# Optimization experiments

Hardware: AMD Instinct MI355X
Metric: run time of the kernel (lower is better)

## Reference

```python
import jax, jax.numpy as jnp
import numpy as np

B, D, H, C, T = 65536, 512, 256, 100, 10
EPS = 0.01  # halt_epsilon


def setup_inputs() -> dict:
    key = jax.random.key(0)
    ks = jax.random.split(key, 10)
    sD = 1.0 / np.sqrt(D)
    sH = 1.0 / np.sqrt(H)
    return {
        "x": jax.random.normal(ks[0], (B, D), dtype=jnp.float32),
        # GRUCell params (PyTorch layout: rows chunked as [r; z; n])
        "W_ih": jax.random.uniform(ks[1], (3 * H, D), minval=-sD, maxval=sD, dtype=jnp.float32),
        "W_hh": jax.random.uniform(ks[2], (3 * H, H), minval=-sH, maxval=sH, dtype=jnp.float32),
        "b_ih": jax.random.uniform(ks[3], (3 * H,), minval=-sH, maxval=sH, dtype=jnp.float32),
        "b_hh": jax.random.uniform(ks[4], (3 * H,), minval=-sH, maxval=sH, dtype=jnp.float32),
        # halting unit
        "W_halt": jax.random.uniform(ks[5], (1, H), minval=-sH, maxval=sH, dtype=jnp.float32),
        "b_halt": jax.random.uniform(ks[6], (1,), minval=-sH, maxval=sH, dtype=jnp.float32),
        # readout
        "W_ro": jax.random.uniform(ks[7], (C, H), minval=-sH, maxval=sH, dtype=jnp.float32),
        "b_ro": jax.random.uniform(ks[8], (C,), minval=-sH, maxval=sH, dtype=jnp.float32),
    }


def _act_forward(x, W_ih, W_hh, b_ih, b_hh, W_halt, b_halt, W_ro, b_ro):
    dt = x.dtype
    thresh = jnp.asarray(1.0 - EPS, dt)
    # x is static across ponder steps -> precompute input projection once
    x_proj = x @ W_ih.T + b_ih                       # [B, 3H]
    xr, xz, xn = jnp.split(x_proj, 3, axis=-1)

    def step(carry, _):
        h, cum, rem, nup, acc = carry
        h_proj = h @ W_hh.T + b_hh                   # [B, 3H]
        hr, hz, hn = jnp.split(h_proj, 3, axis=-1)
        r = jax.nn.sigmoid(xr + hr)
        z = jax.nn.sigmoid(xz + hz)
        n = jnp.tanh(xn + r * hn)
        h_new = (1.0 - z) * n + z * h                # GRUCell update
        halt = jax.nn.sigmoid(h_new @ W_halt.T + b_halt)[:, 0]  # [B]
        logits_t = h_new @ W_ro.T + b_ro             # [B, C]
        still = (cum < thresh).astype(dt)
        new_halt = halt * still
        would = (cum + new_halt > thresh).astype(dt)
        remainder = (1.0 - cum) * would * still
        step_w = new_halt * (1.0 - would) + remainder
        cum2 = cum + step_w
        acc2 = acc + step_w[:, None] * h_new
        return (h_new, cum2, rem + remainder, nup + still, acc2), (h_new, halt, logits_t)

    zB = jnp.zeros((x.shape[0],), dt)
    init = (jnp.zeros((x.shape[0], W_hh.shape[1]), dt), zB, zB, zB,
            jnp.zeros((x.shape[0], W_hh.shape[1]), dt))
    (h, cum, remainders, n_updates, acc), (h_seq, halt_seq, logits_seq) = jax.lax.scan(
        step, init, None, length=T)
    logits = acc @ W_ro.T + b_ro                     # [B, C]
    ponder_cost = n_updates.mean() + remainders.mean()
    # scan stacks on axis 0 (time) -> move to dim 1 as torch.stack(dim=1)
    h_seq = jnp.swapaxes(h_seq, 0, 1)                # [B, T, H]
    halt_seq = jnp.swapaxes(halt_seq, 0, 1)          # [B, T]
    logits_seq = jnp.swapaxes(logits_seq, 0, 1)      # [B, T, C]
    return logits, ponder_cost, n_updates, h_seq, halt_seq, logits_seq


def reference(x, W_ih, W_hh, b_ih, b_hh, W_halt, b_halt, W_ro, b_ro):
    return _act_forward(x, W_ih, W_hh, b_ih, b_hh, W_halt, b_halt, W_ro, b_ro)
```

## Files before the change

kernel.cpp:

```cpp
#include <hip/hip_runtime.h>
#include <cmath>


namespace {
constexpr int B = 65536, D = 512, H = 256, C = 100, T = 10;

constexpr long OUT_LOGITS = 0;
constexpr long OUT_PONDER = (long)B * C;
constexpr long OUT_NUP    = OUT_PONDER + 1;
constexpr long OUT_HSEQ   = OUT_NUP + B;
constexpr long OUT_HALT   = OUT_HSEQ + (long)B * T * H;
constexpr long OUT_LSEQ   = OUT_HALT + (long)B * T;

constexpr long NIH  = 768L * D;
constexpr long NHH  = 768L * H;
constexpr long NAUG = 112L * H;

constexpr long WS_XP   = 0;
constexpr long WS_W16  = WS_XP + (long)B * 768;
constexpr long W_HALV  = 2 * (NIH + NHH + NAUG);
constexpr long WS_HL   = WS_W16 + (W_HALV + 1) / 2;
constexpr long WS_HP4  = WS_HL + (long)B * T;
constexpr long WS_NUPB = WS_HP4 + 4L * B * T;
constexpr long WS_REMB = WS_NUPB + B;
constexpr long WS_H16  = WS_REMB + B;
constexpr long H16_PER_T = 1024L * 32768;

constexpr float SC  = 256.f;
constexpr float ISC = 1.f / 256.f;
constexpr float SB  = 1.f / 65536.f;
}

typedef __attribute__((ext_vector_type(8))) _Float16 h8;
typedef __attribute__((ext_vector_type(4))) _Float16 h4;
typedef __attribute__((ext_vector_type(4))) float f4;

#define MFMA16(A, Bo, Cc) __builtin_amdgcn_mfma_f32_16x16x32_f16(A, Bo, Cc, 0, 0, 0)
#define PROD3(a, Ah, Al, Bh, Bl)                                               \
  a = MFMA16(Al, Bh, a);                                                       \
  a = MFMA16(Ah, Bl, a);                                                       \
  a = MFMA16(Ah, Bh, a);

__device__ __forceinline__ float sigmoidf_(float x) {
  if (x >= 0.f) { return 1.f / (1.f + expf(-x)); }
  float e = expf(x);
  return e / (1.f + e);
}

__device__ __forceinline__ void gload_lds16(const _Float16* g, _Float16* l) {
  __builtin_amdgcn_global_load_lds(
      (const __attribute__((address_space(1))) unsigned int*)g,
      (__attribute__((address_space(3))) unsigned int*)l, 16, 0, 0);
}

__global__ void k_prep(const float* __restrict__ wih_s, const float* __restrict__ whh_s,
                       const float* __restrict__ wro, const float* __restrict__ whalt,
                       _Float16* __restrict__ wr) {
  long idx = (long)blockIdx.x * 256 + threadIdx.x;
  if (idx < NIH) {
    float xs = wih_s[idx] * SC;
    _Float16 h = (_Float16)xs;
    _Float16 l = (_Float16)(xs - (float)h);
    wr[idx] = h; wr[NIH + idx] = l;
  }
  if (idx < NHH) {
    float xs = whh_s[idx] * SC;
    _Float16 h = (_Float16)xs;
    _Float16 l = (_Float16)(xs - (float)h);
    long b = 2 * NIH;
    wr[b + idx] = h; wr[b + NHH + idx] = l;
  }
  if (idx < NAUG) {
    int row = (int)(idx >> 8), k = (int)(idx & 255);
    float x = (row < C) ? wro[row * 256 + k] : ((row == C) ? whalt[k] : 0.f);
    float xs = x * SC;
    _Float16 h = (_Float16)xs;
    _Float16 l = (_Float16)(xs - (float)h);
    long b = 2 * (NIH + NHH);
    wr[b + idx] = h; wr[b + NAUG + idx] = l;
  }
}

__device__ __forceinline__ void stageA16(const float* __restrict__ src,
                                         _Float16* As0, _Float16* As1,
                                         int o) {
#pragma unroll
  for (int i = 0; i < 4; ++i) {
    float4 v = ((const float4*)src)[i];
    float vv[4] = {v.x, v.y, v.z, v.w};
    h4 hh, ll;
#pragma unroll
    for (int c = 0; c < 4; ++c) {
      float sv = vv[c] * SC;
      _Float16 h = (_Float16)sv;
      hh[c] = h;
      ll[c] = (_Float16)(sv - (float)h);
    }
    *(h4*)&As0[o + i * 4] = hh;
    *(h4*)&As1[o + i * 4] = ll;
  }
}

__global__ __launch_bounds__(256, 3) void k_xproj(
    const float* __restrict__ x, const _Float16* __restrict__ wih,
    const float* __restrict__ b_ih, float* __restrict__ xp) {
  __shared__ __align__(16) _Float16 As0[128 * 40], As1[128 * 40];
  __shared__ __align__(16) _Float16 Bs[2][192 * 32];
  const int tid = threadIdx.x;
  const int w = tid >> 6, l = tid & 63;
  const int lr = l & 15, lq = l >> 4;
  const int bid = blockIdx.x;
  const int gid = (bid & 7) * 256 + (bid >> 3);
  const int c0 = (gid & 3) * 64;
  const int rb = (gid >> 2) * 128;

  f4 acc[8][3];
#pragma unroll
  for (int i = 0; i < 8; ++i)
#pragma unroll
    for (int g = 0; g < 3; ++g) acc[i][g] = (f4)0.f;

  for (int kc = 0; kc < 16; ++kc) {
    const int k0 = kc * 32;
    __syncthreads();
    {
      const int row = tid >> 1, kk0 = (tid & 1) * 16;
      stageA16(x + (long)(rb + row) * D + k0 + kk0, As0, As1, row * 40 + kk0);
    }
#pragma unroll
    for (int j = 0; j < 6; ++j) {
      int chunk = w * 6 + j;
      int plane = chunk / 12;
      int rem = chunk - plane * 12;
      int scol = rem * 16 + (l >> 2);
      int kq = l & 3;
      int gcol = (scol >> 6) * 256 + c0 + (scol & 63);
      gload_lds16(wih + (long)plane * NIH + (long)gcol * D + k0 + kq * 8,
                  &Bs[plane][rem * 512]);
    }
    __syncthreads();
    h8 Bh[3], Bl[3];
#pragma unroll
    for (int g = 0; g < 3; ++g) {
      Bh[g] = *(const h8*)&Bs[0][(g * 64 + w * 16 + lr) * 32 + lq * 8];
      Bl[g] = *(const h8*)&Bs[1][(g * 64 + w * 16 + lr) * 32 + lq * 8];
    }
#pragma unroll
    for (int i = 0; i < 8; ++i) {
      h8 Ah = *(const h8*)&As0[(i * 16 + lr) * 40 + lq * 8];
      h8 Al = *(const h8*)&As1[(i * 16 + lr) * 40 + lq * 8];
#pragma unroll
      for (int g = 0; g < 3; ++g) { PROD3(acc[i][g], Ah, Al, Bh[g], Bl[g]); }
    }
  }
  const int ch = c0 + w * 16 + lr;
  float bi[3] = {b_ih[ch], b_ih[256 + ch], b_ih[512 + ch]};
#pragma unroll
  for (int i = 0; i < 8; ++i)
#pragma unroll
    for (int g = 0; g < 3; ++g)
#pragma unroll
      for (int reg = 0; reg < 4; ++reg) {
        long row = rb + i * 16 + lq * 4 + reg;
        xp[row * 768 + g * 256 + ch] = fmaf(acc[i][g][reg], SB, bi[g]);
      }
}

__global__ __launch_bounds__(256, 4) void k_gru(
    const _Float16* __restrict__ whh, const float* __restrict__ xp,
    const float* __restrict__ b_hh, const float* __restrict__ w_halt,
    float* __restrict__ out, _Float16* __restrict__ h16,
    float* __restrict__ hp4, int t) {
  __shared__ __align__(16) _Float16 As[2][64 * 32];
  __shared__ __align__(16) _Float16 Bs[2][192 * 32];
  __shared__ float lds_hp[64][4];
  const int tid = threadIdx.x;
  const int w = tid >> 6, l = tid & 63;
  const int lr = l & 15, lq = l >> 4;
  const int bid = blockIdx.x;
  const int gid = (bid & 7) * 512 + (bid >> 3);
  const int strip = gid & 3;
  const int c0 = strip * 64;
  const int rb = (gid >> 2) * 64;
  const long tilebase = (long)(rb >> 6) * 32768;
  const int ch = c0 + w * 16 + lr;
  const int kc_h = ch >> 5;

  f4 acc[4][3];
  float ho[4][4];
#pragma unroll
  for (int i = 0; i < 4; ++i) {
#pragma unroll
    for (int reg = 0; reg < 4; ++reg) {
      long row = rb + i * 16 + lq * 4 + reg;
      acc[i][0][reg] = xp[row * 768 + ch] * 65536.f;
      acc[i][1][reg] = xp[row * 768 + 256 + ch] * 65536.f;
      ho[i][reg] = 0.f;
    }
    acc[i][2] = (f4)0.f;
  }

  if (t > 0) {
    const _Float16* h16r = h16 + (long)(t - 1) * H16_PER_T + tilebase;
    for (int kc = 0; kc < 8; ++kc) {
      const int k0 = kc * 32;
      __syncthreads();
#pragma unroll
      for (int j = 0; j < 2; ++j) {
        int c = w * 2 + j;
        int plane = c >> 2;
        int cc = c & 3;
        gload_lds16(h16r + (long)kc * 4096 + plane * 2048 + cc * 512 + l * 8,
                    &As[plane][cc * 512]);
      }
#pragma unroll
      for (int j = 0; j < 6; ++j) {
        int chunk = w * 6 + j;
        int plane = chunk / 12;
        int rem = chunk - plane * 12;
        int scol = rem * 16 + (l >> 2);
        int kq = l & 3;
        int gcol = (scol >> 6) * 256 + c0 + (scol & 63);
        gload_lds16(whh + (long)plane * NHH + (long)gcol * H + k0 + kq * 8,
                    &Bs[plane][rem * 512]);
      }
      __syncthreads();
      h8 Bh[3], Bl[3];
#pragma unroll
      for (int g = 0; g < 3; ++g) {
        Bh[g] = *(const h8*)&Bs[0][(g * 64 + w * 16 + lr) * 32 + lq * 8];
        Bl[g] = *(const h8*)&Bs[1][(g * 64 + w * 16 + lr) * 32 + lq * 8];
      }
#pragma unroll
      for (int i = 0; i < 4; ++i) {
        h8 Ah = *(const h8*)&As[0][(i * 16 + lr) * 32 + lq * 8];
        h8 Al = *(const h8*)&As[1][(i * 16 + lr) * 32 + lq * 8];
#pragma unroll
        for (int g = 0; g < 3; ++g) { PROD3(acc[i][g], Ah, Al, Bh[g], Bl[g]); }
      }
      if (kc == kc_h) {
#pragma unroll
        for (int i = 0; i < 4; ++i)
#pragma unroll
          for (int reg = 0; reg < 4; ++reg) {
            int rloc = i * 16 + lq * 4 + reg;
            ho[i][reg] = ((float)As[0][rloc * 32 + (ch & 31)] +
                          (float)As[1][rloc * 32 + (ch & 31)]) * ISC;
          }
      }
    }
  }

  const float bhr = b_hh[ch], bhz = b_hh[256 + ch], bhn = b_hh[512 + ch];
  const float whv = w_halt[ch];
  const long h16base = (long)t * H16_PER_T + tilebase + (long)kc_h * 4096 + (ch & 31);
#pragma unroll
  for (int i = 0; i < 4; ++i)
#pragma unroll
    for (int reg = 0; reg < 4; ++reg) {
      const int rloc = i * 16 + lq * 4 + reg;
      const long row = rb + rloc;
      float xn = xp[row * 768 + 512 + ch];
      float rr = sigmoidf_(fmaf(acc[i][0][reg], SB, bhr));
      float zz = sigmoidf_(fmaf(acc[i][1][reg], SB, bhz));
      float nn = tanhf(xn + rr * fmaf(acc[i][2][reg], SB, bhn));
      float hv = (1.f - zz) * nn + zz * ho[i][reg];
      out[OUT_HSEQ + row * (T * H) + (long)t * H + ch] = hv;
      float sv = hv * SC;
      _Float16 hi = (_Float16)sv;
      _Float16 lo = (_Float16)(sv - (float)hi);
      h16[h16base + (long)rloc * 32] = hi;
      h16[h16base + 2048 + (long)rloc * 32] = lo;
      float p = hv * whv;
#pragma unroll
      for (int m = 1; m < 16; m <<= 1) p += __shfl_xor(p, m, 64);
      if (lr == 0) lds_hp[rloc][w] = p;
    }
  __syncthreads();
  if (tid < 64)
    hp4[((long)t * 4 + strip) * B + rb + tid] =
        ((lds_hp[tid][0] + lds_hp[tid][1]) + (lds_hp[tid][2] + lds_hp[tid][3]));
}

__global__ __launch_bounds__(256, 4) void k_lseq(
    const _Float16* __restrict__ h16, const _Float16* __restrict__ waug,
    const float* __restrict__ b_ro, float* __restrict__ lseq) {
  __shared__ __align__(16) _Float16 As[128 * 32];
  __shared__ __align__(16) _Float16 Bs[112 * 32];
  const int tid = threadIdx.x;
  const int w = tid >> 6, l = tid & 63;
  const int lr = l & 15, lq = l >> 4;
  const int t = blockIdx.x >> 9;
  const int btile = blockIdx.x & 511;
  const _Float16* h16r = h16 + (long)t * H16_PER_T + (long)btile * 65536;

  f4 acc[2][7];
#pragma unroll
  for (int i = 0; i < 2; ++i)
#pragma unroll
    for (int j = 0; j < 7; ++j) acc[i][j] = (f4)0.f;

  for (int kc = 0; kc < 8; ++kc) {
    const int k0 = kc * 32;
    __syncthreads();
#pragma unroll
    for (int j = 0; j < 2; ++j) {
      int c = w * 2 + j;
      gload_lds16(h16r + (long)(c >> 2) * 32768 + (long)kc * 4096 + (c & 3) * 512 + l * 8,
                  &As[c * 512]);
    }
#pragma unroll
    for (int j = 0; j < 2; ++j) {
      int chunk = w + j * 4;
      if (chunk < 7) {
        int scol = chunk * 16 + (l >> 2);
        int kq = l & 3;
        gload_lds16(waug + (long)scol * H + k0 + kq * 8, &Bs[chunk * 512]);
      }
    }
    __syncthreads();
    h8 Af[2];
#pragma unroll
    for (int i = 0; i < 2; ++i)
      Af[i] = *(const h8*)&As[(w * 32 + i * 16 + lr) * 32 + lq * 8];
#pragma unroll
    for (int j = 0; j < 7; ++j) {
      h8 Bf = *(const h8*)&Bs[(j * 16 + lr) * 32 + lq * 8];
#pragma unroll
      for (int i = 0; i < 2; ++i) acc[i][j] = MFMA16(Af[i], Bf, acc[i][j]);
    }
  }
#pragma unroll
  for (int j = 0; j < 7; ++j) {
    const int col = j * 16 + lr;
    if (col < C) {
      const float br = b_ro[col];
#pragma unroll
      for (int i = 0; i < 2; ++i)
#pragma unroll
        for (int reg = 0; reg < 4; ++reg) {
          long b = (long)btile * 128 + w * 32 + i * 16 + lq * 4 + reg;
          lseq[(b * T + t) * C + col] = fmaf(acc[i][j][reg], SB, br);
        }
    }
  }
}

__global__ void k_act(const float* __restrict__ hp4, const float* __restrict__ b_halt,
                      float* __restrict__ out, float* __restrict__ swb,
                      float* __restrict__ nupb, float* __restrict__ remb) {
  const long b = (long)blockIdx.x * 256 + threadIdx.x;
  const float bh = b_halt[0];
  float cum = 0.f, rem = 0.f, nu = 0.f;
#pragma unroll
  for (int t = 0; t < T; ++t) {
    float v = bh + hp4[((long)t * 4 + 0) * B + b] + hp4[((long)t * 4 + 1) * B + b] +
              hp4[((long)t * 4 + 2) * B + b] + hp4[((long)t * 4 + 3) * B + b];
    float halt = sigmoidf_(v);
    out[OUT_HALT + b * T + t] = halt;
    float still = (cum < 0.99f) ? 1.f : 0.f;
    float nh = halt * still;
    float would = ((cum + nh) > 0.99f) ? 1.f : 0.f;
    float rema = (1.f - cum) * would * still;
    float swv = nh * (1.f - would) + rema;
    cum += swv; rem += rema; nu += still;
    swb[b * T + t] = swv;
  }
  nupb[b] = nu; remb[b] = rem;
}

__global__ void k_logits(const float* __restrict__ lseq, const float* __restrict__ swb,
                         const float* __restrict__ b_ro, const float* __restrict__ nupb,
                         float* __restrict__ out) {
  const long b = blockIdx.x;
  const int tid = threadIdx.x;
  if (tid < C) {
    float br = b_ro[tid];
    float s = br;
#pragma unroll
    for (int t = 0; t < T; ++t) {
      float sw = swb[b * T + t];
      s = fmaf(sw, lseq[(b * T + t) * C + tid] - br, s);
    }
    out[OUT_LOGITS + b * C + tid] = s;
  } else if (tid == C) {
    out[OUT_NUP + b] = nupb[b];
  }
}

__global__ void k_ponder(const float* __restrict__ nupb, const float* __restrict__ remb,
                         float* __restrict__ out) {
  __shared__ float sm[4];
  float s = 0.f;
  for (int i = threadIdx.x; i < B; i += 256) s += nupb[i] + remb[i];
#pragma unroll
  for (int m = 1; m < 64; m <<= 1) s += __shfl_xor(s, m, 64);
  int w = threadIdx.x >> 6;
  if ((threadIdx.x & 63) == 0) sm[w] = s;
  __syncthreads();
  if (threadIdx.x == 0)
    out[OUT_PONDER] = (sm[0] + sm[1] + sm[2] + sm[3]) * (1.f / (float)B);
}

extern "C" void kernel_launch(void* const* d_in, const int* in_sizes, int n_in,
                              void* d_out, int out_size, void* d_ws, size_t ws_size,
                              hipStream_t stream) {
  const float* x      = (const float*)d_in[0];
  const float* W_ih   = (const float*)d_in[1];
  const float* W_hh   = (const float*)d_in[2];
  const float* b_ih   = (const float*)d_in[3];
  const float* b_hh   = (const float*)d_in[4];
  const float* W_halt = (const float*)d_in[5];
  const float* b_halt = (const float*)d_in[6];
  const float* W_ro   = (const float*)d_in[7];
  const float* b_ro   = (const float*)d_in[8];
  float* out = (float*)d_out;
  float* ws  = (float*)d_ws;

  float* xp        = ws + WS_XP;
  _Float16* w16    = (_Float16*)(ws + WS_W16);
  _Float16* wih16  = w16;
  _Float16* whh16  = w16 + 2 * NIH;
  _Float16* waug16 = w16 + 2 * (NIH + NHH);
  float* swb  = ws + WS_HL;
  float* hp4  = ws + WS_HP4;
  float* nupb = ws + WS_NUPB;
  float* remb = ws + WS_REMB;
  _Float16* h16 = (_Float16*)(ws + WS_H16);

  k_prep<<<(int)((NIH + 255) / 256), 256, 0, stream>>>(W_ih, W_hh, W_ro, W_halt, w16);
  k_xproj<<<2048, 256, 0, stream>>>(x, wih16, b_ih, xp);
  for (int t = 0; t < T; ++t)
    k_gru<<<4096, 256, 0, stream>>>(whh16, xp, b_hh, W_halt, out, h16, hp4, t);
  k_lseq<<<512 * T, 256, 0, stream>>>(h16, waug16, b_ro, out + OUT_LSEQ);
  k_act<<<B / 256, 256, 0, stream>>>(hp4, b_halt, out, swb, nupb, remb);
  k_logits<<<B, 128, 0, stream>>>(out + OUT_LSEQ, swb, b_ro, nupb, out);
  k_ponder<<<1, 256, 0, stream>>>(nupb, remb, out);
}
```

Measured before the change: 2.192 ms.

## Fuse all GRU timesteps and ACT halting into one persistent row-tile kernel

The ten per-timestep GRU launches are replaced by a single kernel. Each block owns a 64-row tile and loops over all timesteps and all four hidden-column strips, reading back the fp16 hidden state it wrote itself in the previous step. The ACT halting recurrence now runs inside that kernel using shared-memory accumulators, so the separate k_act launch and the hp4 intermediate buffer go away. The aim is to remove launch gaps, tail effects and global round-trips, at the cost of serialising the four column strips within each block and relying on exactly one wave of 1024 resident blocks.

```diff
diff --git a/kernel.cpp b/kernel.cpp
--- a/kernel.cpp
+++ b/kernel.cpp
@@ -20,8 +20,7 @@
 constexpr long WS_W16  = WS_XP + (long)B * 768;
 constexpr long W_HALV  = 2 * (NIH + NHH + NAUG);
 constexpr long WS_HL   = WS_W16 + (W_HALV + 1) / 2;
-constexpr long WS_HP4  = WS_HL + (long)B * T;
-constexpr long WS_NUPB = WS_HP4 + 4L * B * T;
+constexpr long WS_NUPB = WS_HL + (long)B * T;
 constexpr long WS_REMB = WS_NUPB + B;
 constexpr long WS_H16  = WS_REMB + B;
 constexpr long H16_PER_T = 1024L * 32768;
@@ -166,120 +165,154 @@
       }
 }
 
-__global__ __launch_bounds__(256, 4) void k_gru(
+__global__ __launch_bounds__(256, 4) void k_gru_all(
     const _Float16* __restrict__ whh, const float* __restrict__ xp,
     const float* __restrict__ b_hh, const float* __restrict__ w_halt,
-    float* __restrict__ out, _Float16* __restrict__ h16,
-    float* __restrict__ hp4, int t) {
+    const float* __restrict__ b_halt, float* __restrict__ out,
+    _Float16* __restrict__ h16, float* __restrict__ swb,
+    float* __restrict__ nupb, float* __restrict__ remb) {
   __shared__ __align__(16) _Float16 As[2][64 * 32];
   __shared__ __align__(16) _Float16 Bs[2][192 * 32];
   __shared__ float lds_hp[64][4];
+  __shared__ float lds_ss[64][4];
+  __shared__ float lds_cum[64], lds_rem[64], lds_nu[64];
   const int tid = threadIdx.x;
   const int w = tid >> 6, l = tid & 63;
   const int lr = l & 15, lq = l >> 4;
   const int bid = blockIdx.x;
-  const int gid = (bid & 7) * 512 + (bid >> 3);
-  const int strip = gid & 3;
-  const int c0 = strip * 64;
-  const int rb = (gid >> 2) * 64;
-  const long tilebase = (long)(rb >> 6) * 32768;
-  const int ch = c0 + w * 16 + lr;
-  const int kc_h = ch >> 5;
-
-  f4 acc[4][3];
-  float ho[4][4];
-#pragma unroll
-  for (int i = 0; i < 4; ++i) {
-#pragma unroll
-    for (int reg = 0; reg < 4; ++reg) {
-      long row = rb + i * 16 + lq * 4 + reg;
-      acc[i][0][reg] = xp[row * 768 + ch] * 65536.f;
-      acc[i][1][reg] = xp[row * 768 + 256 + ch] * 65536.f;
-      ho[i][reg] = 0.f;
-    }
-    acc[i][2] = (f4)0.f;
-  }
-
-  if (t > 0) {
-    const _Float16* h16r = h16 + (long)(t - 1) * H16_PER_T + tilebase;
-    for (int kc = 0; kc < 8; ++kc) {
-      const int k0 = kc * 32;
+  const int gid = (bid & 7) * 128 + (bid >> 3);
+  const int rb = gid * 64;
+  const long tilebase = (long)gid * 32768;
+  const float bh = b_halt[0];
+
+  if (tid < 64) { lds_cum[tid] = 0.f; lds_rem[tid] = 0.f; lds_nu[tid] = 0.f; }
+
+  for (int t = 0; t < T; ++t) {
+    for (int cs = 0; cs < 4; ++cs) {
+      const int c0 = cs * 64;
+      const int ch = c0 + w * 16 + lr;
+      const int kc_h = ch >> 5;
+
+      f4 acc[4][3];
+      float ho[4][4];
+#pragma unroll
+      for (int i = 0; i < 4; ++i) {
+#pragma unroll
+        for (int reg = 0; reg < 4; ++reg) {
+          long row = rb + i * 16 + lq * 4 + reg;
+          acc[i][0][reg] = xp[row * 768 + ch] * 65536.f;
+          acc[i][1][reg] = xp[row * 768 + 256 + ch] * 65536.f;
+          ho[i][reg] = 0.f;
+        }
+        acc[i][2] = (f4)0.f;
+      }
+
+      if (t > 0) {
+        const _Float16* h16r = h16 + (long)(t - 1) * H16_PER_T + tilebase;
+        for (int kc = 0; kc < 8; ++kc) {
+          const int k0 = kc * 32;
+          __syncthreads();
+#pragma unroll
+          for (int j = 0; j < 2; ++j) {
+            int c = w * 2 + j;
+            int plane = c >> 2;
+            int cc = c & 3;
+            gload_lds16(h16r + (long)kc * 4096 + plane * 2048 + cc * 512 + l * 8,
+                        &As[plane][cc * 512]);
+          }
+#pragma unroll
+          for (int j = 0; j < 6; ++j) {
+            int chunk = w * 6 + j;
+            int plane = chunk / 12;
+            int rem = chunk - plane * 12;
+            int scol = rem * 16 + (l >> 2);
+            int kq = l & 3;
+            int gcol = (scol >> 6) * 256 + c0 + (scol & 63);
+            gload_lds16(whh + (long)plane * NHH + (long)gcol * H + k0 + kq * 8,
+                        &Bs[plane][rem * 512]);
+          }
+          __syncthreads();
+          h8 Bh[3], Bl[3];
+#pragma unroll
+          for (int g = 0; g < 3; ++g) {
+            Bh[g] = *(const h8*)&Bs[0][(g * 64 + w * 16 + lr) * 32 + lq * 8];
+            Bl[g] = *(const h8*)&Bs[1][(g * 64 + w * 16 + lr) * 32 + lq * 8];
+          }
+#pragma unroll
+          for (int i = 0; i < 4; ++i) {
+            h8 Ah = *(const h8*)&As[0][(i * 16 + lr) * 32 + lq * 8];
+            h8 Al = *(const h8*)&As[1][(i * 16 + lr) * 32 + lq * 8];
+#pragma unroll
+            for (int g = 0; g < 3; ++g) { PROD3(acc[i][g], Ah, Al, Bh[g], Bl[g]); }
+          }
+          if (kc == kc_h) {
+#pragma unroll
+            for (int i = 0; i < 4; ++i)
+#pragma unroll
+              for (int reg = 0; reg < 4; ++reg) {
+                int rloc = i * 16 + lq * 4 + reg;
+                ho[i][reg] = ((float)As[0][rloc * 32 + (ch & 31)] +
+                              (float)As[1][rloc * 32 + (ch & 31)]) * ISC;
+              }
+          }
+        }
+      }
+
+      const float bhr = b_hh[ch], bhz = b_hh[256 + ch], bhn = b_hh[512 + ch];
+      const float whv = w_halt[ch];
+      const long h16base = (long)t * H16_PER_T + tilebase + (long)kc_h * 4096 + (ch & 31);
+#pragma unroll
+      for (int i = 0; i < 4; ++i)
+#pragma unroll
+        for (int reg = 0; reg < 4; ++reg) {
+          const int rloc = i * 16 + lq * 4 + reg;
+          const long row = rb + rloc;
+          float xn = xp[row * 768 + 512 + ch];
+          float rr = sigmoidf_(fmaf(acc[i][0][reg], SB, bhr));
+          float zz = sigmoidf_(fmaf(acc[i][1][reg], SB, bhz));
+          float nn = tanhf(xn + rr * fmaf(acc[i][2][reg], SB, bhn));
+          float hv = (1.f - zz) * nn + zz * ho[i][reg];
+          out[OUT_HSEQ + row * (T * H) + (long)t * H + ch] = hv;
+          float sv = hv * SC;
+          _Float16 hi = (_Float16)sv;
+          _Float16 lo = (_Float16)(sv - (float)hi);
+          h16[h16base + (long)rloc * 32] = hi;
+          h16[h16base + 2048 + (long)rloc * 32] = lo;
+          float p = hv * whv;
+#pragma unroll
+          for (int m = 1; m < 16; m <<= 1) p += __shfl_xor(p, m, 64);
+          if (lr == 0) lds_hp[rloc][w] = p;
+        }
       __syncthreads();
-#pragma unroll
-      for (int j = 0; j < 2; ++j) {
-        int c = w * 2 + j;
-        int plane = c >> 2;
-        int cc = c & 3;
-        gload_lds16(h16r + (long)kc * 4096 + plane * 2048 + cc * 512 + l * 8,
-                    &As[plane][cc * 512]);
-      }
-#pragma unroll
-      for (int j = 0; j < 6; ++j) {
-        int chunk = w * 6 + j;
-        int plane = chunk / 12;
-        int rem = chunk - plane * 12;
-        int scol = rem * 16 + (l >> 2);
-        int kq = l & 3;
-        int gcol = (scol >> 6) * 256 + c0 + (scol & 63);
-        gload_lds16(whh + (long)plane * NHH + (long)gcol * H + k0 + kq * 8,
-                    &Bs[plane][rem * 512]);
-      }
+      if (tid < 64)
+        lds_ss[tid][cs] =
+            (lds_hp[tid][0] + lds_hp[tid][1]) + (lds_hp[tid][2] + lds_hp[tid][3]);
       __syncthreads();
-      h8 Bh[3], Bl[3];
-#pragma unroll
-      for (int g = 0; g < 3; ++g) {
-        Bh[g] = *(const h8*)&Bs[0][(g * 64 + w * 16 + lr) * 32 + lq * 8];
-        Bl[g] = *(const h8*)&Bs[1][(g * 64 + w * 16 + lr) * 32 + lq * 8];
-      }
-#pragma unroll
-      for (int i = 0; i < 4; ++i) {
-        h8 Ah = *(const h8*)&As[0][(i * 16 + lr) * 32 + lq * 8];
-        h8 Al = *(const h8*)&As[1][(i * 16 + lr) * 32 + lq * 8];
-#pragma unroll
-        for (int g = 0; g < 3; ++g) { PROD3(acc[i][g], Ah, Al, Bh[g], Bl[g]); }
-      }
-      if (kc == kc_h) {
-#pragma unroll
-        for (int i = 0; i < 4; ++i)
-#pragma unroll
-          for (int reg = 0; reg < 4; ++reg) {
-            int rloc = i * 16 + lq * 4 + reg;
-            ho[i][reg] = ((float)As[0][rloc * 32 + (ch & 31)] +
-                          (float)As[1][rloc * 32 + (ch & 31)]) * ISC;
-          }
-      }
-    }
-  }
-
-  const float bhr = b_hh[ch], bhz = b_hh[256 + ch], bhn = b_hh[512 + ch];
-  const float whv = w_halt[ch];
-  const long h16base = (long)t * H16_PER_T + tilebase + (long)kc_h * 4096 + (ch & 31);
-#pragma unroll
-  for (int i = 0; i < 4; ++i)
-#pragma unroll
-    for (int reg = 0; reg < 4; ++reg) {
-      const int rloc = i * 16 + lq * 4 + reg;
-      const long row = rb + rloc;
-      float xn = xp[row * 768 + 512 + ch];
-      float rr = sigmoidf_(fmaf(acc[i][0][reg], SB, bhr));
-      float zz = sigmoidf_(fmaf(acc[i][1][reg], SB, bhz));
-      float nn = tanhf(xn + rr * fmaf(acc[i][2][reg], SB, bhn));
-      float hv = (1.f - zz) * nn + zz * ho[i][reg];
-      out[OUT_HSEQ + row * (T * H) + (long)t * H + ch] = hv;
-      float sv = hv * SC;
-      _Float16 hi = (_Float16)sv;
-      _Float16 lo = (_Float16)(sv - (float)hi);
-      h16[h16base + (long)rloc * 32] = hi;
-      h16[h16base + 2048 + (long)rloc * 32] = lo;
-      float p = hv * whv;
-#pragma unroll
-      for (int m = 1; m < 16; m <<= 1) p += __shfl_xor(p, m, 64);
-      if (lr == 0) lds_hp[rloc][w] = p;
-    }
-  __syncthreads();
-  if (tid < 64)
-    hp4[((long)t * 4 + strip) * B + rb + tid] =
-        ((lds_hp[tid][0] + lds_hp[tid][1]) + (lds_hp[tid][2] + lds_hp[tid][3]));
+    }
+
+    if (tid < 64) {
+      const long b = rb + tid;
+      float v = bh + lds_ss[tid][0] + lds_ss[tid][1] + lds_ss[tid][2] + lds_ss[tid][3];
+      float halt = sigmoidf_(v);
+      out[OUT_HALT + b * T + t] = halt;
+      float cum = lds_cum[tid];
+      float still = (cum < 0.99f) ? 1.f : 0.f;
+      float nh = halt * still;
+      float would = ((cum + nh) > 0.99f) ? 1.f : 0.f;
+      float rema = (1.f - cum) * would * still;
+      float swv = nh * (1.f - would) + rema;
+      lds_cum[tid] = cum + swv;
+      lds_rem[tid] += rema;
+      lds_nu[tid] += still;
+      swb[b * T + t] = swv;
+    }
+    __syncthreads();
+  }
+
+  if (tid < 64) {
+    nupb[rb + tid] = lds_nu[tid];
+    remb[rb + tid] = lds_rem[tid];
+  }
 }
 
 __global__ __launch_bounds__(256, 4) void k_lseq(
@@ -344,29 +377,6 @@
         }
     }
   }
-}
-
-__global__ void k_act(const float* __restrict__ hp4, const float* __restrict__ b_halt,
-                      float* __restrict__ out, float* __restrict__ swb,
-                      float* __restrict__ nupb, float* __restrict__ remb) {
-  const long b = (long)blockIdx.x * 256 + threadIdx.x;
-  const float bh = b_halt[0];
-  float cum = 0.f, rem = 0.f, nu = 0.f;
-#pragma unroll
-  for (int t = 0; t < T; ++t) {
-    float v = bh + hp4[((long)t * 4 + 0) * B + b] + hp4[((long)t * 4 + 1) * B + b] +
-              hp4[((long)t * 4 + 2) * B + b] + hp4[((long)t * 4 + 3) * B + b];
-    float halt = sigmoidf_(v);
-    out[OUT_HALT + b * T + t] = halt;
-    float still = (cum < 0.99f) ? 1.f : 0.f;
-    float nh = halt * still;
-    float would = ((cum + nh) > 0.99f) ? 1.f : 0.f;
-    float rema = (1.f - cum) * would * still;
-    float swv = nh * (1.f - would) + rema;
-    cum += swv; rem += rema; nu += still;
-    swb[b * T + t] = swv;
-  }
-  nupb[b] = nu; remb[b] = rem;
 }
 
 __global__ void k_logits(const float* __restrict__ lseq, const float* __restrict__ swb,
@@ -423,17 +433,15 @@
   _Float16* whh16  = w16 + 2 * NIH;
   _Float16* waug16 = w16 + 2 * (NIH + NHH);
   float* swb  = ws + WS_HL;
-  float* hp4  = ws + WS_HP4;
   float* nupb = ws + WS_NUPB;
   float* remb = ws + WS_REMB;
   _Float16* h16 = (_Float16*)(ws + WS_H16);
 
   k_prep<<<(int)((NIH + 255) / 256), 256, 0, stream>>>(W_ih, W_hh, W_ro, W_halt, w16);
   k_xproj<<<2048, 256, 0, stream>>>(x, wih16, b_ih, xp);
-  for (int t = 0; t < T; ++t)
-    k_gru<<<4096, 256, 0, stream>>>(whh16, xp, b_hh, W_halt, out, h16, hp4, t);
+  k_gru_all<<<1024, 256, 0, stream>>>(whh16, xp, b_hh, W_halt, b_halt, out, h16,
+                                      swb, nupb, remb);
   k_lseq<<<512 * T, 256, 0, stream>>>(h16, waug16, b_ro, out + OUT_LSEQ);
-  k_act<<<B / 256, 256, 0, stream>>>(hp4, b_halt, out, swb, nupb, remb);
   k_logits<<<B, 128, 0, stream>>>(out + OUT_LSEQ, swb, b_ro, nupb, out);
   k_ponder<<<1, 256, 0, stream>>>(nupb, remb, out);
 }
```

Result: slower. 4.029 ms (+83.8%).

## Fuse logits-seq GEMM with weighted logits reduction and swizzle LDS layouts

Applied to the files above, without the earlier changes.

Replaces the separate per-timestep readout GEMM and the logits reduction kernel with one kernel that loops over all timesteps per 64-row tile. It accumulates the step-weighted logits in registers, which avoids re-reading the large logits sequence. The nupdate output moves into the ACT kernel. Separately, it applies an XOR swizzle to the LDS layouts of the xproj, GRU and readout GEMMs to reduce bank conflicts on fragment reads. The fused kernel launches only 1024 blocks and runs the timesteps serially, which may reduce parallelism.

```diff
diff --git a/kernel.cpp b/kernel.cpp
--- a/kernel.cpp
+++ b/kernel.cpp
@@ -40,6 +40,9 @@
   a = MFMA16(Al, Bh, a);                                                       \
   a = MFMA16(Ah, Bl, a);                                                       \
   a = MFMA16(Ah, Bh, a);
+
+#define SWZ_L(l)  ((((l) & 3) ^ (((l) >> 3) & 3)) << 3)
+#define SWZ_RD(lq, lr) (((lq) ^ (((lr) >> 1) & 3)) << 3)
 
 __device__ __forceinline__ float sigmoidf_(float x) {
   if (x >= 0.f) { return 1.f / (1.f + expf(-x)); }
@@ -133,17 +136,16 @@
       int plane = chunk / 12;
       int rem = chunk - plane * 12;
       int scol = rem * 16 + (l >> 2);
-      int kq = l & 3;
       int gcol = (scol >> 6) * 256 + c0 + (scol & 63);
-      gload_lds16(wih + (long)plane * NIH + (long)gcol * D + k0 + kq * 8,
+      gload_lds16(wih + (long)plane * NIH + (long)gcol * D + k0 + SWZ_L(l),
                   &Bs[plane][rem * 512]);
     }
     __syncthreads();
     h8 Bh[3], Bl[3];
 #pragma unroll
     for (int g = 0; g < 3; ++g) {
-      Bh[g] = *(const h8*)&Bs[0][(g * 64 + w * 16 + lr) * 32 + lq * 8];
-      Bl[g] = *(const h8*)&Bs[1][(g * 64 + w * 16 + lr) * 32 + lq * 8];
+      Bh[g] = *(const h8*)&Bs[0][(g * 64 + w * 16 + lr) * 32 + SWZ_RD(lq, lr)];
+      Bl[g] = *(const h8*)&Bs[1][(g * 64 + w * 16 + lr) * 32 + SWZ_RD(lq, lr)];
     }
 #pragma unroll
     for (int i = 0; i < 8; ++i) {
@@ -210,7 +212,8 @@
         int c = w * 2 + j;
         int plane = c >> 2;
         int cc = c & 3;
-        gload_lds16(h16r + (long)kc * 4096 + plane * 2048 + cc * 512 + l * 8,
+        gload_lds16(h16r + (long)kc * 4096 + plane * 2048 + cc * 512 +
+                        (l >> 2) * 32 + SWZ_L(l),
                     &As[plane][cc * 512]);
       }
 #pragma unroll
@@ -219,22 +222,21 @@
         int plane = chunk / 12;
         int rem = chunk - plane * 12;
         int scol = rem * 16 + (l >> 2);
-        int kq = l & 3;
         int gcol = (scol >> 6) * 256 + c0 + (scol & 63);
-        gload_lds16(whh + (long)plane * NHH + (long)gcol * H + k0 + kq * 8,
+        gload_lds16(whh + (long)plane * NHH + (long)gcol * H + k0 + SWZ_L(l),
                     &Bs[plane][rem * 512]);
       }
       __syncthreads();
       h8 Bh[3], Bl[3];
 #pragma unroll
       for (int g = 0; g < 3; ++g) {
-        Bh[g] = *(const h8*)&Bs[0][(g * 64 + w * 16 + lr) * 32 + lq * 8];
-        Bl[g] = *(const h8*)&Bs[1][(g * 64 + w * 16 + lr) * 32 + lq * 8];
+        Bh[g] = *(const h8*)&Bs[0][(g * 64 + w * 16 + lr) * 32 + SWZ_RD(lq, lr)];
+        Bl[g] = *(const h8*)&Bs[1][(g * 64 + w * 16 + lr) * 32 + SWZ_RD(lq, lr)];
       }
 #pragma unroll
       for (int i = 0; i < 4; ++i) {
-        h8 Ah = *(const h8*)&As[0][(i * 16 + lr) * 32 + lq * 8];
-        h8 Al = *(const h8*)&As[1][(i * 16 + lr) * 32 + lq * 8];
+        h8 Ah = *(const h8*)&As[0][(i * 16 + lr) * 32 + SWZ_RD(lq, lr)];
+        h8 Al = *(const h8*)&As[1][(i * 16 + lr) * 32 + SWZ_RD(lq, lr)];
 #pragma unroll
         for (int g = 0; g < 3; ++g) { PROD3(acc[i][g], Ah, Al, Bh[g], Bl[g]); }
       }
@@ -244,8 +246,9 @@
 #pragma unroll
           for (int reg = 0; reg < 4; ++reg) {
             int rloc = i * 16 + lq * 4 + reg;
-            ho[i][reg] = ((float)As[0][rloc * 32 + (ch & 31)] +
-                          (float)As[1][rloc * 32 + (ch & 31)]) * ISC;
+            int sl = ((((ch >> 3) & 3) ^ ((rloc >> 1) & 3)) << 3) + (ch & 7);
+            ho[i][reg] = ((float)As[0][rloc * 32 + sl] +
+                          (float)As[1][rloc * 32 + sl]) * ISC;
           }
       }
     }
@@ -282,70 +285,6 @@
         ((lds_hp[tid][0] + lds_hp[tid][1]) + (lds_hp[tid][2] + lds_hp[tid][3]));
 }
 
-__global__ __launch_bounds__(256, 4) void k_lseq(
-    const _Float16* __restrict__ h16, const _Float16* __restrict__ waug,
-    const float* __restrict__ b_ro, float* __restrict__ lseq) {
-  __shared__ __align__(16) _Float16 As[128 * 32];
-  __shared__ __align__(16) _Float16 Bs[112 * 32];
-  const int tid = threadIdx.x;
-  const int w = tid >> 6, l = tid & 63;
-  const int lr = l & 15, lq = l >> 4;
-  const int t = blockIdx.x >> 9;
-  const int btile = blockIdx.x & 511;
-  const _Float16* h16r = h16 + (long)t * H16_PER_T + (long)btile * 65536;
-
-  f4 acc[2][7];
-#pragma unroll
-  for (int i = 0; i < 2; ++i)
-#pragma unroll
-    for (int j = 0; j < 7; ++j) acc[i][j] = (f4)0.f;
-
-  for (int kc = 0; kc < 8; ++kc) {
-    const int k0 = kc * 32;
-    __syncthreads();
-#pragma unroll
-    for (int j = 0; j < 2; ++j) {
-      int c = w * 2 + j;
-      gload_lds16(h16r + (long)(c >> 2) * 32768 + (long)kc * 4096 + (c & 3) * 512 + l * 8,
-                  &As[c * 512]);
-    }
-#pragma unroll
-    for (int j = 0; j < 2; ++j) {
-      int chunk = w + j * 4;
-      if (chunk < 7) {
-        int scol = chunk * 16 + (l >> 2);
-        int kq = l & 3;
-        gload_lds16(waug + (long)scol * H + k0 + kq * 8, &Bs[chunk * 512]);
-      }
-    }
-    __syncthreads();
-    h8 Af[2];
-#pragma unroll
-    for (int i = 0; i < 2; ++i)
-      Af[i] = *(const h8*)&As[(w * 32 + i * 16 + lr) * 32 + lq * 8];
-#pragma unroll
-    for (int j = 0; j < 7; ++j) {
-      h8 Bf = *(const h8*)&Bs[(j * 16 + lr) * 32 + lq * 8];
-#pragma unroll
-      for (int i = 0; i < 2; ++i) acc[i][j] = MFMA16(Af[i], Bf, acc[i][j]);
-    }
-  }
-#pragma unroll
-  for (int j = 0; j < 7; ++j) {
-    const int col = j * 16 + lr;
-    if (col < C) {
-      const float br = b_ro[col];
-#pragma unroll
-      for (int i = 0; i < 2; ++i)
-#pragma unroll
-        for (int reg = 0; reg < 4; ++reg) {
-          long b = (long)btile * 128 + w * 32 + i * 16 + lq * 4 + reg;
-          lseq[(b * T + t) * C + col] = fmaf(acc[i][j][reg], SB, br);
-        }
-    }
-  }
-}
-
 __global__ void k_act(const float* __restrict__ hp4, const float* __restrict__ b_halt,
                       float* __restrict__ out, float* __restrict__ swb,
                       float* __restrict__ nupb, float* __restrict__ remb) {
@@ -367,24 +306,84 @@
     swb[b * T + t] = swv;
   }
   nupb[b] = nu; remb[b] = rem;
-}
-
-__global__ void k_logits(const float* __restrict__ lseq, const float* __restrict__ swb,
-                         const float* __restrict__ b_ro, const float* __restrict__ nupb,
-                         float* __restrict__ out) {
-  const long b = blockIdx.x;
+  out[OUT_NUP + b] = nu;
+}
+
+__global__ __launch_bounds__(256, 4) void k_lseq2(
+    const _Float16* __restrict__ h16, const _Float16* __restrict__ waug,
+    const float* __restrict__ b_ro, const float* __restrict__ swb,
+    float* __restrict__ out) {
+  __shared__ __align__(16) _Float16 As[64 * 32];
+  __shared__ __align__(16) _Float16 Bs[112 * 32];
+  __shared__ float swf[640];
   const int tid = threadIdx.x;
-  if (tid < C) {
-    float br = b_ro[tid];
-    float s = br;
-#pragma unroll
-    for (int t = 0; t < T; ++t) {
-      float sw = swb[b * T + t];
-      s = fmaf(sw, lseq[(b * T + t) * C + tid] - br, s);
-    }
-    out[OUT_LOGITS + b * C + tid] = s;
-  } else if (tid == C) {
-    out[OUT_NUP + b] = nupb[b];
+  const int w = tid >> 6, l = tid & 63;
+  const int lr = l & 15, lq = l >> 4;
+  const long rb = (long)blockIdx.x * 64;
+  const long tilebase = (long)blockIdx.x * 32768;
+
+  for (int j = tid; j < 640; j += 256) swf[j] = swb[rb * T + j];
+
+  float br_[7];
+#pragma unroll
+  for (int j = 0; j < 7; ++j) {
+    int col = j * 16 + lr;
+    br_[j] = (col < C) ? b_ro[col] : 0.f;
+  }
+
+  f4 Lacc[7];
+#pragma unroll
+  for (int j = 0; j < 7; ++j) Lacc[j] = (f4)0.f;
+
+  for (int t = 0; t < T; ++t) {
+    const _Float16* h16t = h16 + (long)t * H16_PER_T + tilebase;
+    f4 acc[7];
+#pragma unroll
+    for (int j = 0; j < 7; ++j) acc[j] = (f4)0.f;
+
+    for (int kc = 0; kc < 8; ++kc) {
+      __syncthreads();
+      gload_lds16(h16t + (long)kc * 4096 + w * 512 + (l >> 2) * 32 + SWZ_L(l),
+                  &As[w * 512]);
+#pragma unroll
+      for (int j = 0; j < 2; ++j) {
+        int chunk = w + j * 4;
+        if (chunk < 7) {
+          int scol = chunk * 16 + (l >> 2);
+          gload_lds16(waug + (long)scol * H + kc * 32 + SWZ_L(l), &Bs[chunk * 512]);
+        }
+      }
+      __syncthreads();
+      h8 Af = *(const h8*)&As[(w * 16 + lr) * 32 + SWZ_RD(lq, lr)];
+#pragma unroll
+      for (int j = 0; j < 7; ++j) {
+        h8 Bf = *(const h8*)&Bs[(j * 16 + lr) * 32 + SWZ_RD(lq, lr)];
+        acc[j] = MFMA16(Af, Bf, acc[j]);
+      }
+    }
+#pragma unroll
+    for (int reg = 0; reg < 4; ++reg) {
+      const long m = rb + w * 16 + lq * 4 + reg;
+      const float swv = swf[(w * 16 + lq * 4 + reg) * 10 + t];
+#pragma unroll
+      for (int j = 0; j < 7; ++j) {
+        int col = j * 16 + lr;
+        if (col < C) {
+          out[OUT_LSEQ + (m * T + t) * C + col] = fmaf(acc[j][reg], SB, br_[j]);
+          Lacc[j][reg] = fmaf(swv, acc[j][reg], Lacc[j][reg]);
+        }
+      }
+    }
+  }
+#pragma unroll
+  for (int reg = 0; reg < 4; ++reg) {
+    const long m = rb + w * 16 + lq * 4 + reg;
+#pragma unroll
+    for (int j = 0; j < 7; ++j) {
+      int col = j * 16 + lr;
+      if (col < C)
+        out[OUT_LOGITS + m * C + col] = fmaf(Lacc[j][reg], SB, br_[j]);
+    }
   }
 }
 
@@ -432,8 +431,7 @@
   k_xproj<<<2048, 256, 0, stream>>>(x, wih16, b_ih, xp);
   for (int t = 0; t < T; ++t)
     k_gru<<<4096, 256, 0, stream>>>(whh16, xp, b_hh, W_halt, out, h16, hp4, t);
-  k_lseq<<<512 * T, 256, 0, stream>>>(h16, waug16, b_ro, out + OUT_LSEQ);
   k_act<<<B / 256, 256, 0, stream>>>(hp4, b_halt, out, swb, nupb, remb);
-  k_logits<<<B, 128, 0, stream>>>(out + OUT_LSEQ, swb, b_ro, nupb, out);
+  k_lseq2<<<1024, 256, 0, stream>>>(h16, waug16, b_ro, swb, out);
   k_ponder<<<1, 256, 0, stream>>>(nupb, remb, out);
 }
```

Measured after the change: 3.314 ms. 51.2% more time.

## Store input projection in MFMA-fragment-tiled layout for vectorized GRU loads

Applied to the files above, without the earlier changes.

The input projection buffer is rewritten in a tiled layout that matches the accumulator fragment ownership of each thread, so k_xproj writes float4s and k_gru reads r/z/n gate inputs as three float4 loads per row group. Before, each thread did scalar strided loads across 768-wide rows in every one of the ten GRU step launches. The n-gate input is now loaded up front into registers rather than in the epilogue, which raises register pressure slightly. Producer and consumer index maps must agree exactly.

```diff
diff --git a/kernel.cpp b/kernel.cpp
--- a/kernel.cpp
+++ b/kernel.cpp
@@ -103,7 +103,7 @@
 
 __global__ __launch_bounds__(256, 3) void k_xproj(
     const float* __restrict__ x, const _Float16* __restrict__ wih,
-    const float* __restrict__ b_ih, float* __restrict__ xp) {
+    const float* __restrict__ b_ih, float* __restrict__ xpt) {
   __shared__ __align__(16) _Float16 As0[128 * 40], As1[128 * 40];
   __shared__ __align__(16) _Float16 Bs[2][192 * 32];
   const int tid = threadIdx.x;
@@ -154,20 +154,25 @@
     }
   }
   const int ch = c0 + w * 16 + lr;
+  const int strip = gid & 3;
   float bi[3] = {b_ih[ch], b_ih[256 + ch], b_ih[512 + ch]};
-#pragma unroll
-  for (int i = 0; i < 8; ++i)
-#pragma unroll
-    for (int g = 0; g < 3; ++g)
-#pragma unroll
-      for (int reg = 0; reg < 4; ++reg) {
-        long row = rb + i * 16 + lq * 4 + reg;
-        xp[row * 768 + g * 256 + ch] = fmaf(acc[i][g][reg], SB, bi[g]);
-      }
+  const long xoff = (long)(lq * 256 + w * 64 + lr * 4);
+#pragma unroll
+  for (int i = 0; i < 8; ++i) {
+    const long t4s = (long)((gid >> 2) * 2 + (i >> 2)) * 4 + strip;
+#pragma unroll
+    for (int g = 0; g < 3; ++g) {
+      float4 v = make_float4(fmaf(acc[i][g][0], SB, bi[g]),
+                             fmaf(acc[i][g][1], SB, bi[g]),
+                             fmaf(acc[i][g][2], SB, bi[g]),
+                             fmaf(acc[i][g][3], SB, bi[g]));
+      *(float4*)&xpt[((t4s * 3 + g) * 4 + (i & 3)) * 1024 + xoff] = v;
+    }
+  }
 }
 
 __global__ __launch_bounds__(256, 4) void k_gru(
-    const _Float16* __restrict__ whh, const float* __restrict__ xp,
+    const _Float16* __restrict__ whh, const float* __restrict__ xpt,
     const float* __restrict__ b_hh, const float* __restrict__ w_halt,
     float* __restrict__ out, _Float16* __restrict__ h16,
     float* __restrict__ hp4, int t) {
@@ -188,16 +193,22 @@
 
   f4 acc[4][3];
   float ho[4][4];
+  float xnv[4][4];
+  const long t4s = (long)(gid >> 2) * 4 + strip;
+  const long xoff = (long)(lq * 256 + w * 64 + lr * 4);
 #pragma unroll
   for (int i = 0; i < 4; ++i) {
-#pragma unroll
-    for (int reg = 0; reg < 4; ++reg) {
-      long row = rb + i * 16 + lq * 4 + reg;
-      acc[i][0][reg] = xp[row * 768 + ch] * 65536.f;
-      acc[i][1][reg] = xp[row * 768 + 256 + ch] * 65536.f;
-      ho[i][reg] = 0.f;
-    }
+    float4 vr = *(const float4*)&xpt[((t4s * 3 + 0) * 4 + i) * 1024 + xoff];
+    float4 vz = *(const float4*)&xpt[((t4s * 3 + 1) * 4 + i) * 1024 + xoff];
+    float4 vn = *(const float4*)&xpt[((t4s * 3 + 2) * 4 + i) * 1024 + xoff];
+    acc[i][0][0] = vr.x * 65536.f; acc[i][0][1] = vr.y * 65536.f;
+    acc[i][0][2] = vr.z * 65536.f; acc[i][0][3] = vr.w * 65536.f;
+    acc[i][1][0] = vz.x * 65536.f; acc[i][1][1] = vz.y * 65536.f;
+    acc[i][1][2] = vz.z * 65536.f; acc[i][1][3] = vz.w * 65536.f;
+    xnv[i][0] = vn.x; xnv[i][1] = vn.y; xnv[i][2] = vn.z; xnv[i][3] = vn.w;
     acc[i][2] = (f4)0.f;
+#pragma unroll
+    for (int reg = 0; reg < 4; ++reg) ho[i][reg] = 0.f;
   }
 
   if (t > 0) {
@@ -260,10 +271,9 @@
     for (int reg = 0; reg < 4; ++reg) {
       const int rloc = i * 16 + lq * 4 + reg;
       const long row = rb + rloc;
-      float xn = xp[row * 768 + 512 + ch];
       float rr = sigmoidf_(fmaf(acc[i][0][reg], SB, bhr));
       float zz = sigmoidf_(fmaf(acc[i][1][reg], SB, bhz));
-      float nn = tanhf(xn + rr * fmaf(acc[i][2][reg], SB, bhn));
+      float nn = tanhf(xnv[i][reg] + rr * fmaf(acc[i][2][reg], SB, bhn));
       float hv = (1.f - zz) * nn + zz * ho[i][reg];
       out[OUT_HSEQ + row * (T * H) + (long)t * H + ch] = hv;
       float sv = hv * SC;
@@ -417,7 +427,7 @@
   float* out = (float*)d_out;
   float* ws  = (float*)d_ws;
 
-  float* xp        = ws + WS_XP;
+  float* xpt       = ws + WS_XP;
   _Float16* w16    = (_Float16*)(ws + WS_W16);
   _Float16* wih16  = w16;
   _Float16* whh16  = w16 + 2 * NIH;
@@ -429,9 +439,9 @@
   _Float16* h16 = (_Float16*)(ws + WS_H16);
 
   k_prep<<<(int)((NIH + 255) / 256), 256, 0, stream>>>(W_ih, W_hh, W_ro, W_halt, w16);
-  k_xproj<<<2048, 256, 0, stream>>>(x, wih16, b_ih, xp);
+  k_xproj<<<2048, 256, 0, stream>>>(x, wih16, b_ih, xpt);
   for (int t = 0; t < T; ++t)
-    k_gru<<<4096, 256, 0, stream>>>(whh16, xp, b_hh, W_halt, out, h16, hp4, t);
+    k_gru<<<4096, 256, 0, stream>>>(whh16, xpt, b_hh, W_halt, out, h16, hp4, t);
   k_lseq<<<512 * T, 256, 0, stream>>>(h16, waug16, b_ro, out + OUT_LSEQ);
   k_act<<<B / 256, 256, 0, stream>>>(hp4, b_halt, out, swb, nupb, remb);
   k_logits<<<B, 128, 0, stream>>>(out + OUT_LSEQ, swb, b_ro, nupb, out);
```

Result: no change. 2.189 ms (-0.2%).
